# Optimization experiments

Measured on AMD Instinct MI355X. Metric: run time of the kernel, lower is better.

## Reference

```python
import jax, jax.numpy as jnp
import numpy as np

N_DET, N_T, NY, NX, B = 128, 2048, 256, 256, 4


def setup_inputs() -> dict:
    key = jax.random.key(0)
    k1, k2, k3 = jax.random.split(key, 3)
    sino = jax.random.normal(k1, (B, 1, N_DET, N_T), dtype=jnp.float32)
    # lut[..., 0]: fractional time-of-flight index in [0, n_t-1)
    tof = jax.random.uniform(k2, (NY, NX, N_DET), dtype=jnp.float32) * (N_T - 1)
    # lut[..., 1]: linear-interp fraction alpha in [0, 1)
    alpha = jax.random.uniform(k3, (NY, NX, N_DET), dtype=jnp.float32)
    lut = jnp.stack([tof, alpha], axis=-1)  # [ny, nx, n_det, 2]
    return {"sino": sino, "lut": lut}


def reference(sino, lut):
    b, _, n_det, n_t = sino.shape
    ny, nx = lut.shape[0], lut.shape[1]
    P = ny * nx

    # Precompute (as in __init__): floor index, validity mask, interp fraction.
    k_floor = jnp.floor(lut[..., 0])
    valid = (k_floor >= 0) & (k_floor < n_t - 1)
    k0 = jnp.clip(k_floor, 0, max(n_t - 2, 0)).astype(jnp.int32)  # [ny,nx,n_det]
    alpha = lut[..., 1]

    # Hann apodization window over detectors (non-trainable buffer).
    apod = (0.5 - 0.5 * jnp.cos(
        2.0 * jnp.pi * jnp.arange(n_det, dtype=jnp.float32) / max(n_det - 1, 1)
    )).astype(sino.dtype)

    S = sino[:, 0]  # [B, n_det, n_t]

    # Move detector axis first so we can gather all detectors at once.
    k0t = k0.reshape(P, n_det).T          # [n_det, P]
    at = alpha.reshape(P, n_det).T        # [n_det, P]
    vt = valid.reshape(P, n_det).T.astype(sino.dtype)  # [n_det, P]

    s0 = jnp.take_along_axis(S, k0t[None], axis=2)        # [B, n_det, P]
    s1 = jnp.take_along_axis(S, (k0t + 1)[None], axis=2)  # [B, n_det, P]
    sk = ((1.0 - at) * s0 + at * s1) * vt                  # masked lerp

    out = jnp.einsum('d,bdp->bp', apod, sk)                # apodized reduce over detectors
    norm = jnp.maximum(apod.sum(), jnp.finfo(apod.dtype).tiny)
    return (out / norm).reshape(b, 1, ny, nx)
```

## Files before the change

### kernel.cpp

```cpp
#include <hip/hip_runtime.h>
#include <hip/hip_fp16.h>

#define N_DET 128
#define N_T   2048
#define NPIX  65536
#define NBATCH 4

typedef float f4_t __attribute__((ext_vector_type(4)));
typedef f4_t __attribute__((aligned(8))) f4a8_t;

__global__ __launch_bounds__(256) void sino_pack_kernel(
    const float* __restrict__ sino, float2* __restrict__ ws) {
  const int idx = blockIdx.x * blockDim.x + threadIdx.x;
  const __half2 lo = __floats2half2_rn(
      __builtin_nontemporal_load(sino + 0 * N_DET * N_T + idx),
      __builtin_nontemporal_load(sino + 1 * N_DET * N_T + idx));
  const __half2 hi = __floats2half2_rn(
      __builtin_nontemporal_load(sino + 2 * N_DET * N_T + idx),
      __builtin_nontemporal_load(sino + 3 * N_DET * N_T + idx));
  union { struct { __half2 a, b; } h; float2 f; } u;
  u.h.a = lo;
  u.h.b = hi;
  ws[idx] = u.f;
}

__global__ __launch_bounds__(256) void das_packed_kernel(
    const float* __restrict__ lut, const unsigned char* __restrict__ S8,
    float* __restrict__ out) {
  const int lane = threadIdx.x & 63;
  const int p = blockIdx.x * 4 + (threadIdx.x >> 6);

  const f4_t lv = __builtin_nontemporal_load(
      reinterpret_cast<const f4_t*>(lut + (size_t)p * 2 * N_DET) + lane);

  float acc0 = 0.f, acc1 = 0.f, acc2 = 0.f, acc3 = 0.f;
  float wsum = 0.f;

#pragma unroll
  for (int j = 0; j < 2; ++j) {
    const int d = 2 * lane + j;
    const float tof = j ? lv.z : lv.x;
    const float a   = j ? lv.w : lv.y;

    const float kf = floorf(tof);
    const bool valid = (kf >= 0.0f) && (kf < (float)(N_T - 1));
    const float kcl = fminf(fmaxf(kf, 0.0f), (float)(N_T - 2));
    const int k0 = (int)kcl;

    const float apd =
        0.5f - 0.5f * cosf(6.28318530717958647692f *
                           (1.0f / (float)(N_DET - 1)) * (float)d);
    wsum += apd;
    const float w = valid ? apd : 0.0f;
    const float om = 1.0f - a;

    const f4a8_t v = *reinterpret_cast<const f4a8_t*>(
        S8 + ((size_t)d * N_T + k0) * 8);
    const __half2* hp = reinterpret_cast<const __half2*>(&v);
    const float2 s0a = __half22float2(hp[0]);
    const float2 s0b = __half22float2(hp[1]);
    const float2 s1a = __half22float2(hp[2]);
    const float2 s1b = __half22float2(hp[3]);

    acc0 += w * (om * s0a.x + a * s1a.x);
    acc1 += w * (om * s0a.y + a * s1a.y);
    acc2 += w * (om * s0b.x + a * s1b.x);
    acc3 += w * (om * s0b.y + a * s1b.y);
  }

#pragma unroll
  for (int off = 32; off > 0; off >>= 1) {
    acc0 += __shfl_xor(acc0, off);
    acc1 += __shfl_xor(acc1, off);
    acc2 += __shfl_xor(acc2, off);
    acc3 += __shfl_xor(acc3, off);
    wsum += __shfl_xor(wsum, off);
  }

  if (lane == 0) {
    const float inv = 1.0f / fmaxf(wsum, 1.17549435e-38f);
    __builtin_nontemporal_store(acc0 * inv, out + 0 * NPIX + p);
    __builtin_nontemporal_store(acc1 * inv, out + 1 * NPIX + p);
    __builtin_nontemporal_store(acc2 * inv, out + 2 * NPIX + p);
    __builtin_nontemporal_store(acc3 * inv, out + 3 * NPIX + p);
  }
}

__global__ __launch_bounds__(256) void das_fallback_kernel(
    const float* __restrict__ lut, const float* __restrict__ S,
    float* __restrict__ out) {
  const int lane = threadIdx.x & 63;
  const int p = blockIdx.x * 4 + (threadIdx.x >> 6);

  const float4 lv =
      reinterpret_cast<const float4*>(lut + (size_t)p * 2 * N_DET)[lane];

  float acc0 = 0.f, acc1 = 0.f, acc2 = 0.f, acc3 = 0.f;
  float wsum = 0.f;

#pragma unroll
  for (int j = 0; j < 2; ++j) {
    const int d = 2 * lane + j;
    const float tof = j ? lv.z : lv.x;
    const float a   = j ? lv.w : lv.y;
    const float kf = floorf(tof);
    const bool valid = (kf >= 0.0f) && (kf < (float)(N_T - 1));
    const float kcl = fminf(fmaxf(kf, 0.0f), (float)(N_T - 2));
    const int k0 = (int)kcl;
    const float apd =
        0.5f - 0.5f * cosf(6.28318530717958647692f *
                           (1.0f / (float)(N_DET - 1)) * (float)d);
    wsum += apd;
    const float w = valid ? apd : 0.0f;
    const float om = 1.0f - a;
    const float* row = S + (size_t)d * N_T + k0;
    acc0 += w * (om * row[0 * N_DET * N_T] + a * row[0 * N_DET * N_T + 1]);
    acc1 += w * (om * row[1 * N_DET * N_T] + a * row[1 * N_DET * N_T + 1]);
    acc2 += w * (om * row[2 * N_DET * N_T] + a * row[2 * N_DET * N_T + 1]);
    acc3 += w * (om * row[3 * N_DET * N_T] + a * row[3 * N_DET * N_T + 1]);
  }

#pragma unroll
  for (int off = 32; off > 0; off >>= 1) {
    acc0 += __shfl_xor(acc0, off);
    acc1 += __shfl_xor(acc1, off);
    acc2 += __shfl_xor(acc2, off);
    acc3 += __shfl_xor(acc3, off);
    wsum += __shfl_xor(wsum, off);
  }

  if (lane == 0) {
    const float inv = 1.0f / fmaxf(wsum, 1.17549435e-38f);
    out[0 * NPIX + p] = acc0 * inv;
    out[1 * NPIX + p] = acc1 * inv;
    out[2 * NPIX + p] = acc2 * inv;
    out[3 * NPIX + p] = acc3 * inv;
  }
}

extern "C" void kernel_launch(void* const* d_in, const int* in_sizes, int n_in,
                              void* d_out, int out_size, void* d_ws, size_t ws_size,
                              hipStream_t stream) {
  const float* sino = (const float*)d_in[0];
  const float* lut  = (const float*)d_in[1];
  float* out = (float*)d_out;

  const size_t need = (size_t)N_DET * N_T * 8;
  if (ws_size >= need) {
    float2* ws = (float2*)d_ws;
    sino_pack_kernel<<<(N_DET * N_T) / 256, 256, 0, stream>>>(sino, ws);
    das_packed_kernel<<<NPIX / 4, 256, 0, stream>>>(
        lut, (const unsigned char*)d_ws, out);
  } else {
    das_fallback_kernel<<<NPIX / 4, 256, 0, stream>>>(lut, sino, out);
  }
}
```

Measured before the change: 141.2 us.

## Map one pixel per thread with detector groups and LDS reduction

Restructures the DAS kernel so each thread handles one pixel over a 32-detector slice, with four slices per block combined through shared memory. Apodization weights are computed once into LDS and the normalization is folded into a constant, removing per-element cosf and shuffle reductions. The trade-off is that lookup-table reads become strided across lanes, which may hurt coalescing of the dominant memory stream.

Result: faster. 133.9 us (-5.2%).

```diff
diff --git a/kernel.cpp b/kernel.cpp
--- a/kernel.cpp
+++ b/kernel.cpp
@@ -5,6 +5,9 @@
 #define N_T   2048
 #define NPIX  65536
 #define NBATCH 4
+#define PIX_PER_BLK 64
+#define NGRP 4
+#define DETS_PER_GRP 32
 
 typedef float f4_t __attribute__((ext_vector_type(4)));
 typedef f4_t __attribute__((aligned(8))) f4a8_t;
@@ -24,66 +27,71 @@
   ws[idx] = u.f;
 }
 
-__global__ __launch_bounds__(256) void das_packed_kernel(
+__global__ __launch_bounds__(256) void das_kernel(
     const float* __restrict__ lut, const unsigned char* __restrict__ S8,
     float* __restrict__ out) {
-  const int lane = threadIdx.x & 63;
-  const int p = blockIdx.x * 4 + (threadIdx.x >> 6);
+  __shared__ float apod_s[N_DET];
+  __shared__ float red[NGRP][PIX_PER_BLK][NBATCH];
 
-  const f4_t lv = __builtin_nontemporal_load(
-      reinterpret_cast<const f4_t*>(lut + (size_t)p * 2 * N_DET) + lane);
+  const int x = threadIdx.x;
+  const int y = threadIdx.y;
+  const int tid = y * PIX_PER_BLK + x;
+  const int p = blockIdx.x * PIX_PER_BLK + x;
 
-  float acc0 = 0.f, acc1 = 0.f, acc2 = 0.f, acc3 = 0.f;
-  float wsum = 0.f;
+  if (tid < N_DET) {
+    apod_s[tid] = 0.5f - 0.5f * cosf(6.28318530717958647692f *
+                                     ((float)tid / (float)(N_DET - 1)));
+  }
+  __syncthreads();
+
+  const float* lutp = lut + ((size_t)p * N_DET + y * DETS_PER_GRP) * 2;
+  const int dbase0 = y * DETS_PER_GRP;
+
+  float a0 = 0.f, a1 = 0.f, a2 = 0.f, a3 = 0.f;
+
+#pragma unroll 2
+  for (int c = 0; c < DETS_PER_GRP / 4; ++c) {
+    const f4_t l0 = *reinterpret_cast<const f4_t*>(lutp + c * 8);
+    const f4_t l1 = *reinterpret_cast<const f4_t*>(lutp + c * 8 + 4);
+    const float tofs[4] = {l0.x, l0.z, l1.x, l1.z};
+    const float als[4]  = {l0.y, l0.w, l1.y, l1.w};
+    const int dbase = dbase0 + c * 4;
+
+    f4_t v[4];
+    float kfs[4];
+#pragma unroll
+    for (int j = 0; j < 4; ++j) {
+      const float kf = floorf(tofs[j]);
+      kfs[j] = kf;
+      const float kcl = fminf(fmaxf(kf, 0.0f), (float)(N_T - 2));
+      const unsigned k0 = (unsigned)(int)kcl;
+      const unsigned voff = ((unsigned)(dbase + j) * N_T + k0) * 8u;
+      v[j] = *reinterpret_cast<const f4a8_t*>(S8 + voff);
+    }
 
 #pragma unroll
-  for (int j = 0; j < 2; ++j) {
-    const int d = 2 * lane + j;
-    const float tof = j ? lv.z : lv.x;
-    const float a   = j ? lv.w : lv.y;
-
-    const float kf = floorf(tof);
-    const bool valid = (kf >= 0.0f) && (kf < (float)(N_T - 1));
-    const float kcl = fminf(fmaxf(kf, 0.0f), (float)(N_T - 2));
-    const int k0 = (int)kcl;
-
-    const float apd =
-        0.5f - 0.5f * cosf(6.28318530717958647692f *
-                           (1.0f / (float)(N_DET - 1)) * (float)d);
-    wsum += apd;
-    const float w = valid ? apd : 0.0f;
-    const float om = 1.0f - a;
-
-    const f4a8_t v = *reinterpret_cast<const f4a8_t*>(
-        S8 + ((size_t)d * N_T + k0) * 8);
-    const __half2* hp = reinterpret_cast<const __half2*>(&v);
-    const float2 s0a = __half22float2(hp[0]);
-    const float2 s0b = __half22float2(hp[1]);
-    const float2 s1a = __half22float2(hp[2]);
-    const float2 s1b = __half22float2(hp[3]);
-
-    acc0 += w * (om * s0a.x + a * s1a.x);
-    acc1 += w * (om * s0a.y + a * s1a.y);
-    acc2 += w * (om * s0b.x + a * s1b.x);
-    acc3 += w * (om * s0b.y + a * s1b.y);
+    for (int j = 0; j < 4; ++j) {
+      const bool valid = (kfs[j] >= 0.0f) && (kfs[j] < (float)(N_T - 1));
+      const float w = valid ? apod_s[dbase + j] : 0.0f;
+      const float al = als[j];
+      const __half2* hp = reinterpret_cast<const __half2*>(&v[j]);
+      const float2 s0a = __half22float2(hp[0]);
+      const float2 s0b = __half22float2(hp[1]);
+      const float2 s1a = __half22float2(hp[2]);
+      const float2 s1b = __half22float2(hp[3]);
+      a0 += w * (s0a.x + al * (s1a.x - s0a.x));
+      a1 += w * (s0a.y + al * (s1a.y - s0a.y));
+      a2 += w * (s0b.x + al * (s1b.x - s0b.x));
+      a3 += w * (s0b.y + al * (s1b.y - s0b.y));
+    }
   }
 
-#pragma unroll
-  for (int off = 32; off > 0; off >>= 1) {
-    acc0 += __shfl_xor(acc0, off);
-    acc1 += __shfl_xor(acc1, off);
-    acc2 += __shfl_xor(acc2, off);
-    acc3 += __shfl_xor(acc3, off);
-    wsum += __shfl_xor(wsum, off);
-  }
+  *reinterpret_cast<float4*>(&red[y][x][0]) = make_float4(a0, a1, a2, a3);
+  __syncthreads();
 
-  if (lane == 0) {
-    const float inv = 1.0f / fmaxf(wsum, 1.17549435e-38f);
-    __builtin_nontemporal_store(acc0 * inv, out + 0 * NPIX + p);
-    __builtin_nontemporal_store(acc1 * inv, out + 1 * NPIX + p);
-    __builtin_nontemporal_store(acc2 * inv, out + 2 * NPIX + p);
-    __builtin_nontemporal_store(acc3 * inv, out + 3 * NPIX + p);
-  }
+  const float s = red[0][x][y] + red[1][x][y] + red[2][x][y] + red[3][x][y];
+  __builtin_nontemporal_store(s * (1.0f / 63.5f),
+                              out + (size_t)y * NPIX + blockIdx.x * PIX_PER_BLK + x);
 }
 
 __global__ __launch_bounds__(256) void das_fallback_kernel(
@@ -149,7 +157,8 @@
   if (ws_size >= need) {
     float2* ws = (float2*)d_ws;
     sino_pack_kernel<<<(N_DET * N_T) / 256, 256, 0, stream>>>(sino, ws);
-    das_packed_kernel<<<NPIX / 4, 256, 0, stream>>>(
+    dim3 blk(PIX_PER_BLK, NGRP);
+    das_kernel<<<NPIX / PIX_PER_BLK, blk, 0, stream>>>(
         lut, (const unsigned char*)d_ws, out);
   } else {
     das_fallback_kernel<<<NPIX / 4, 256, 0, stream>>>(lut, sino, out);
```

## Stage detector-group sinogram slices in LDS and split-reduce over detectors with atomics

Applied to the files above, without the earlier changes.

Replaces the one-wavefront-per-pixel gather kernel with a 2D grid over pixel tiles and groups of 8 detectors. Each block copies a 128KB fp16-packed sinogram slice into shared memory, then serves the interpolation gathers from LDS instead of scattered global loads. Partial sums are combined with float atomicAdd into an output zeroed by an added memset, and the apodization normalization becomes a constant. The trade-offs are lower occupancy from the large LDS footprint, repeated slice loads per block, uncoalesced strided LUT reads, and 16 atomics per output element.

Result: faster. 121.7 us (-13.8%).

```diff
diff --git a/kernel.cpp b/kernel.cpp
--- a/kernel.cpp
+++ b/kernel.cpp
@@ -5,9 +5,11 @@
 #define N_T   2048
 #define NPIX  65536
 #define NBATCH 4
+#define G 8
+#define PT 1024
+#define NGB (N_DET / G)
 
 typedef float f4_t __attribute__((ext_vector_type(4)));
-typedef f4_t __attribute__((aligned(8))) f4a8_t;
 
 __global__ __launch_bounds__(256) void sino_pack_kernel(
     const float* __restrict__ sino, float2* __restrict__ ws) {
@@ -24,65 +26,73 @@
   ws[idx] = u.f;
 }
 
-__global__ __launch_bounds__(256) void das_packed_kernel(
-    const float* __restrict__ lut, const unsigned char* __restrict__ S8,
+__global__ __launch_bounds__(256) void das_lds_kernel(
+    const float* __restrict__ lut, const float2* __restrict__ ws,
     float* __restrict__ out) {
-  const int lane = threadIdx.x & 63;
-  const int p = blockIdx.x * 4 + (threadIdx.x >> 6);
+  __shared__ float2 sino_s[G * N_T];
 
-  const f4_t lv = __builtin_nontemporal_load(
-      reinterpret_cast<const f4_t*>(lut + (size_t)p * 2 * N_DET) + lane);
+  const int tid = threadIdx.x;
+  const int tile = blockIdx.x;
+  const int g = blockIdx.y;
 
-  float acc0 = 0.f, acc1 = 0.f, acc2 = 0.f, acc3 = 0.f;
-  float wsum = 0.f;
+  f4_t l[PT / 256][4];
+#pragma unroll
+  for (int i = 0; i < PT / 256; ++i) {
+    const int p = tile * PT + i * 256 + tid;
+    const f4_t* lp =
+        reinterpret_cast<const f4_t*>(lut + ((size_t)p * N_DET + g * G) * 2);
+#pragma unroll
+    for (int j = 0; j < 4; ++j) l[i][j] = lp[j];
+  }
+
+  {
+    const float4* src = reinterpret_cast<const float4*>(ws + (size_t)g * G * N_T);
+    float4* dst = reinterpret_cast<float4*>(sino_s);
+#pragma unroll
+    for (int i = 0; i < 8192 / 256; ++i) dst[tid + i * 256] = src[tid + i * 256];
+  }
+
+  float apd[G];
+#pragma unroll
+  for (int j = 0; j < G; ++j) {
+    apd[j] = 0.5f - 0.5f * cosf(6.28318530717958647692f *
+                                ((float)(g * G + j) / (float)(N_DET - 1)));
+  }
+  __syncthreads();
 
 #pragma unroll
-  for (int j = 0; j < 2; ++j) {
-    const int d = 2 * lane + j;
-    const float tof = j ? lv.z : lv.x;
-    const float a   = j ? lv.w : lv.y;
+  for (int i = 0; i < PT / 256; ++i) {
+    const int p = tile * PT + i * 256 + tid;
+    float a0 = 0.f, a1 = 0.f, a2 = 0.f, a3 = 0.f;
+#pragma unroll
+    for (int j = 0; j < G; ++j) {
+      const float tof = (j & 1) ? l[i][j >> 1].z : l[i][j >> 1].x;
+      const float al  = (j & 1) ? l[i][j >> 1].w : l[i][j >> 1].y;
+      const float kf = floorf(tof);
+      const bool valid = (kf >= 0.0f) && (kf < (float)(N_T - 1));
+      const float kcl = fminf(fmaxf(kf, 0.0f), (float)(N_T - 2));
+      const int k0 = (int)kcl;
+      const float w = valid ? apd[j] : 0.0f;
 
-    const float kf = floorf(tof);
-    const bool valid = (kf >= 0.0f) && (kf < (float)(N_T - 1));
-    const float kcl = fminf(fmaxf(kf, 0.0f), (float)(N_T - 2));
-    const int k0 = (int)kcl;
+      const float2 r0 = sino_s[j * N_T + k0];
+      const float2 r1 = sino_s[j * N_T + k0 + 1];
+      const __half2* h0 = reinterpret_cast<const __half2*>(&r0);
+      const __half2* h1 = reinterpret_cast<const __half2*>(&r1);
+      const float2 s0a = __half22float2(h0[0]);
+      const float2 s0b = __half22float2(h0[1]);
+      const float2 s1a = __half22float2(h1[0]);
+      const float2 s1b = __half22float2(h1[1]);
 
-    const float apd =
-        0.5f - 0.5f * cosf(6.28318530717958647692f *
-                           (1.0f / (float)(N_DET - 1)) * (float)d);
-    wsum += apd;
-    const float w = valid ? apd : 0.0f;
-    const float om = 1.0f - a;
-
-    const f4a8_t v = *reinterpret_cast<const f4a8_t*>(
-        S8 + ((size_t)d * N_T + k0) * 8);
-    const __half2* hp = reinterpret_cast<const __half2*>(&v);
-    const float2 s0a = __half22float2(hp[0]);
-    const float2 s0b = __half22float2(hp[1]);
-    const float2 s1a = __half22float2(hp[2]);
-    const float2 s1b = __half22float2(hp[3]);
-
-    acc0 += w * (om * s0a.x + a * s1a.x);
-    acc1 += w * (om * s0a.y + a * s1a.y);
-    acc2 += w * (om * s0b.x + a * s1b.x);
-    acc3 += w * (om * s0b.y + a * s1b.y);
-  }
-
-#pragma unroll
-  for (int off = 32; off > 0; off >>= 1) {
-    acc0 += __shfl_xor(acc0, off);
-    acc1 += __shfl_xor(acc1, off);
-    acc2 += __shfl_xor(acc2, off);
-    acc3 += __shfl_xor(acc3, off);
-    wsum += __shfl_xor(wsum, off);
-  }
-
-  if (lane == 0) {
-    const float inv = 1.0f / fmaxf(wsum, 1.17549435e-38f);
-    __builtin_nontemporal_store(acc0 * inv, out + 0 * NPIX + p);
-    __builtin_nontemporal_store(acc1 * inv, out + 1 * NPIX + p);
-    __builtin_nontemporal_store(acc2 * inv, out + 2 * NPIX + p);
-    __builtin_nontemporal_store(acc3 * inv, out + 3 * NPIX + p);
+      a0 += w * (s0a.x + al * (s1a.x - s0a.x));
+      a1 += w * (s0a.y + al * (s1a.y - s0a.y));
+      a2 += w * (s0b.x + al * (s1b.x - s0b.x));
+      a3 += w * (s0b.y + al * (s1b.y - s0b.y));
+    }
+    const float nrm = 1.0f / 63.5f;
+    atomicAdd(out + 0 * NPIX + p, a0 * nrm);
+    atomicAdd(out + 1 * NPIX + p, a1 * nrm);
+    atomicAdd(out + 2 * NPIX + p, a2 * nrm);
+    atomicAdd(out + 3 * NPIX + p, a3 * nrm);
   }
 }
 
@@ -147,10 +157,11 @@
 
   const size_t need = (size_t)N_DET * N_T * 8;
   if (ws_size >= need) {
+    hipMemsetAsync(d_out, 0, (size_t)out_size * sizeof(float), stream);
     float2* ws = (float2*)d_ws;
     sino_pack_kernel<<<(N_DET * N_T) / 256, 256, 0, stream>>>(sino, ws);
-    das_packed_kernel<<<NPIX / 4, 256, 0, stream>>>(
-        lut, (const unsigned char*)d_ws, out);
+    dim3 grid(NPIX / PT, NGB);
+    das_lds_kernel<<<grid, 256, 0, stream>>>(lut, ws, out);
   } else {
     das_fallback_kernel<<<NPIX / 4, 256, 0, stream>>>(lut, sino, out);
   }
```
